# Optimization experiments

Hardware: AMD Instinct MI355X
Metric: run time of the kernel (lower is better)

Reference implementation:

```python
import jax, jax.numpy as jnp
import numpy as np

B, N, DQ, DK, DV, H = 8, 1024, 512, 512, 512, 8
DH = DV // H  # 64


def setup_inputs() -> dict:
    key = jax.random.key(0)
    ks = jax.random.split(key, 12)
    Q = jax.random.normal(ks[0], (B, N, DQ), jnp.float32)
    K = jax.random.normal(ks[1], (B, N, DK), jnp.float32)
    U = jax.random.normal(ks[2], (H, N, N, B), jnp.float32) * 0.1  # additive bias, [H,Nq,Nk,B]
    mask = (jax.random.uniform(ks[3], (B, N)) < 0.9).astype(jnp.float32)
    w = 0.02
    return {
        'Q': Q, 'K': K, 'U': U, 'mask': mask,
        'Wq': jax.random.normal(ks[4], (DQ, DV), jnp.float32) * w,
        'bq': jnp.zeros((DV,), jnp.float32),
        'Wk': jax.random.normal(ks[5], (DK, DV), jnp.float32) * w,
        'bk': jnp.zeros((DV,), jnp.float32),
        'Wv': jax.random.normal(ks[6], (DK, DV), jnp.float32) * w,
        'bv': jnp.zeros((DV,), jnp.float32),
        'Wo': jax.random.normal(ks[7], (DV, DV), jnp.float32) * w,
        'bo': jnp.zeros((DV,), jnp.float32),
    }


def reference(Q, K, U, mask, Wq, bq, Wk, bk, Wv, bv, Wo, bo):
    m = mask[:, :, None]  # [B,N,1]
    q = (Q @ Wq + bq) * m  # [B,N,DV]
    k = (K @ Wk + bk) * m
    v = (K @ Wv + bv) * m
    # split heads: torch.cat(split(dh,2),0) is head-major -> [H,B,N,DH]
    qh = q.reshape(B, N, H, DH).transpose(2, 0, 1, 3)
    kh = k.reshape(B, N, H, DH).transpose(2, 0, 1, 3)
    vh = v.reshape(B, N, H, DH).transpose(2, 0, 1, 3)
    # U.transpose(1,3).transpose(-1,-2).reshape(H*B,N,N) == transpose(U,(0,3,1,2))
    bias = jnp.transpose(U, (0, 3, 1, 2))  # [H,B,Nq,Nk]
    scores = jnp.einsum('hbid,hbjd->hbij', qh, kh) / np.sqrt(DV) + bias
    # custom double-masked softmax (max taken over unmasked scores, faithfully)
    max_elem = jnp.max(scores, axis=3, keepdims=True)
    m1 = mask[None, :, :, None]  # [1,B,Nq,1]
    m2 = mask[None, :, None, :]  # [1,B,1,Nk]
    num = jnp.exp((scores - max_elem) * m1 * m2) * m1 * m2
    A = num / (jnp.sum(num, axis=3, keepdims=True) + 1e-16)
    o = qh + jnp.einsum('hbij,hbjd->hbid', A, vh)  # residual, [H,B,N,DH]
    O = o.transpose(1, 2, 0, 3).reshape(B, N, DV)  # merge heads
    O = O + jax.nn.relu((O @ Wo + bo) * m)
    return O
```

## Files before the change

kernel.cpp:

```cpp
#include <hip/hip_runtime.h>

#define B_   8
#define N_   1024
#define D_   512
#define H_   8
#define DH_  64
#define SCALE_ 0.044194173824159216f
#define LOG2E_ 1.4426950408889634f

typedef __attribute__((ext_vector_type(8))) short bf16x8;
typedef __attribute__((ext_vector_type(4))) float f32x4;
typedef __attribute__((ext_vector_type(8))) unsigned short us8;

__device__ __forceinline__ unsigned short f2bf(float f) {
  unsigned u = __builtin_bit_cast(unsigned, f);
  u += 0x7fffu + ((u >> 16) & 1u);
  return (unsigned short)(u >> 16);
}
__device__ __forceinline__ float bf2f(unsigned short h) {
  unsigned u = ((unsigned)h) << 16;
  return __builtin_bit_cast(float, u);
}
__device__ __forceinline__ void gl_lds16(const void* g, void* l) {
  __builtin_amdgcn_global_load_lds(
      (const __attribute__((address_space(1))) unsigned int*)g,
      (__attribute__((address_space(3))) unsigned int*)l, 16, 0, 0);
}
#define MFMA16(a, b, c) __builtin_amdgcn_mfma_f32_16x16x32_bf16((a), (b), (c), 0, 0, 0)

__global__ void prep_w(const float* __restrict__ Wq, const float* __restrict__ Wk,
                       const float* __restrict__ Wv, const float* __restrict__ Wo,
                       unsigned short* __restrict__ WT) {
  int idx = blockIdx.x * 256 + threadIdx.x;
  int mat = idx >> 18;
  int rem = idx & 0x3FFFF;
  int k = rem >> 9, n = rem & 511;
  const float* W = (mat == 0) ? Wq : (mat == 1) ? Wk : (mat == 2) ? Wv : Wo;
  float v = W[(size_t)k * 512 + n];
  int kmap = (k & ~63) | ((k & 63) ^ ((n & 7) << 3));
  WT[(size_t)mat * 262144 + (size_t)n * 512 + kmap] = f2bf(v);
}

#define GEMM_BODY(A, W, bias, EPILOGUE)                                          \
  __shared__ unsigned short Alds[2][128][72];                                    \
  __shared__ unsigned short Blds[2][128 * 64];                                   \
  const int t = threadIdx.x, w = t >> 6, l = t & 63;                             \
  const int wr = w >> 1, wc = w & 1;                                             \
  const int lm = l & 15, lg = l >> 4;                                            \
  const int bm = blockIdx.x >> 2, bn = blockIdx.x & 3;                           \
  f32x4 acc[4][4];                                                               \
  _Pragma("unroll") for (int mt = 0; mt < 4; ++mt)                               \
  _Pragma("unroll") for (int nt = 0; nt < 4; ++nt)                               \
      acc[mt][nt] = f32x4{0.f, 0.f, 0.f, 0.f};                                   \
  float4 areg[8];                                                                \
  auto loadA = [&](int kt) {                                                     \
    _Pragma("unroll") for (int p = 0; p < 8; ++p) {                              \
      int row = (t >> 4) + p * 16, col = (t & 15) * 4;                           \
      areg[p] = *(const float4*)&A[((size_t)(bm * 128 + row)) * 512 + kt * 64 + col]; \
    }                                                                            \
  };                                                                             \
  auto issueB = [&](int kt, int sb) {                                            \
    _Pragma("unroll") for (int p = 0; p < 4; ++p) {                              \
      int chunk = w * 4 + p;                                                     \
      int row = chunk * 8 + (l >> 3), gc = kt * 64 + (l & 7) * 8;                \
      gl_lds16(&W[((size_t)(bn * 128 + row)) * 512 + gc],                        \
               &Blds[sb][chunk * 512 + l * 8]);                                  \
    }                                                                            \
  };                                                                             \
  auto writeA = [&](int sb) {                                                    \
    _Pragma("unroll") for (int p = 0; p < 8; ++p) {                              \
      int row = (t >> 4) + p * 16, col = (t & 15) * 4;                           \
      float4 v = areg[p];                                                        \
      uint2 d;                                                                   \
      d.x = (unsigned)f2bf(v.x) | ((unsigned)f2bf(v.y) << 16);                   \
      d.y = (unsigned)f2bf(v.z) | ((unsigned)f2bf(v.w) << 16);                   \
      *(uint2*)&Alds[sb][row][col] = d;                                          \
    }                                                                            \
  };                                                                             \
  loadA(0); issueB(0, 0); writeA(0);                                             \
  __syncthreads();                                                               \
  int buf = 0;                                                                   \
  for (int kt = 0; kt < 8; ++kt) {                                               \
    if (kt + 1 < 8) { loadA(kt + 1); issueB(kt + 1, buf ^ 1); }                  \
    _Pragma("unroll") for (int kk = 0; kk < 2; ++kk) {                           \
      bf16x8 af[4], bfv[4];                                                      \
      _Pragma("unroll") for (int mt = 0; mt < 4; ++mt)                           \
        af[mt] = *(const bf16x8*)&Alds[buf][wr * 64 + mt * 16 + lm][kk * 32 + lg * 8]; \
      _Pragma("unroll") for (int nt = 0; nt < 4; ++nt) {                         \
        int rr = wc * 64 + nt * 16 + lm;                                         \
        int c = (kk * 32 + lg * 8) ^ ((rr & 7) << 3);                            \
        bfv[nt] = *(const bf16x8*)&Blds[buf][rr * 64 + c];                       \
      }                                                                          \
      _Pragma("unroll") for (int mt = 0; mt < 4; ++mt)                           \
      _Pragma("unroll") for (int nt = 0; nt < 4; ++nt)                           \
          acc[mt][nt] = MFMA16(af[mt], bfv[nt], acc[mt][nt]);                    \
    }                                                                            \
    if (kt + 1 < 8) writeA(buf ^ 1);                                             \
    __syncthreads();                                                             \
    buf ^= 1;                                                                    \
  }                                                                              \
  _Pragma("unroll") for (int mt = 0; mt < 4; ++mt)                               \
  _Pragma("unroll") for (int nt = 0; nt < 4; ++nt) {                             \
    int gn = bn * 128 + wc * 64 + nt * 16 + lm;                                  \
    float bv_ = bias[gn];                                                        \
    _Pragma("unroll") for (int e = 0; e < 4; ++e) {                              \
      int gm = bm * 128 + wr * 64 + mt * 16 + lg * 4 + e;                        \
      float v = acc[mt][nt][e] + bv_;                                            \
      size_t off = (size_t)gm * 512 + gn;                                        \
      EPILOGUE                                                                   \
    }                                                                            \
  }

__global__ __launch_bounds__(256, 2) void gemm_proj3(
    const float* __restrict__ Q, const float* __restrict__ K,
    const unsigned short* __restrict__ WT,
    const float* __restrict__ bq, const float* __restrict__ bk,
    const float* __restrict__ bv, const float* __restrict__ mask,
    unsigned short* __restrict__ qb, unsigned short* __restrict__ kb,
    unsigned short* __restrict__ vtmp) {
  const int mat = blockIdx.y;
  const float* A = (mat == 0) ? Q : K;
  const unsigned short* W = WT + (size_t)mat * 262144;
  const float* bias = (mat == 0) ? bq : (mat == 1) ? bk : bv;
  unsigned short* outp = (mat == 0) ? qb : (mat == 1) ? kb : vtmp;
  GEMM_BODY(A, W, bias, { outp[off] = f2bf(v * mask[gm]); })
}

__global__ __launch_bounds__(256, 2) void gemm_final(
    const float* __restrict__ A, const unsigned short* __restrict__ W,
    const float* __restrict__ bias, const float* __restrict__ mask,
    const float* __restrict__ resid, float* __restrict__ outp) {
  GEMM_BODY(A, W, bias, { outp[off] = resid[off] + fmaxf(v, 0.f) * mask[gm]; })
}

__global__ void vtrans_kernel(const unsigned short* __restrict__ vtmp,
                              unsigned short* __restrict__ vT) {
  __shared__ unsigned short T[64][72];
  int b = blockIdx.x, ntile = blockIdx.y, dtile = blockIdx.z;
  int n0 = ntile * 64, d0 = dtile * 64;
  int t = threadIdx.x;
#pragma unroll
  for (int p = 0; p < 2; ++p) {
    int r = (t >> 3) + p * 32;
    int c = (t & 7) * 8;
    *(us8*)&T[r][c] = *(const us8*)&vtmp[((size_t)(b * N_ + n0 + r)) * D_ + d0 + c];
  }
  __syncthreads();
#pragma unroll
  for (int p = 0; p < 2; ++p) {
    int r = (t >> 3) + p * 32;
    int c = (t & 7) * 8;
    us8 v;
#pragma unroll
    for (int e = 0; e < 8; ++e) v[e] = T[c + e][r];
    *(us8*)&vT[((size_t)(b * D_ + d0 + r)) * N_ + n0 + c] = v;
  }
}

__global__ __launch_bounds__(512, 2) void attn_kernel(
    const unsigned short* __restrict__ qb, const unsigned short* __restrict__ kb,
    const unsigned short* __restrict__ vT, const float* __restrict__ U,
    const float* __restrict__ mask, float* __restrict__ O32) {
  __shared__ float Ulds[2][32 * 256];
  __shared__ float Plds[8][32 * 36];
  const int t = threadIdx.x, w = t >> 6, l = t & 63;
  const int h = blockIdx.x >> 5;
  const int i0 = (blockIdx.x & 31) * 32;
  const int b = w;
  const int lm = l & 15, lg = l >> 4;
  const int bh = b >> 2;
  const int xw_b = (b & 3) ^ (lm & 3);

  float4 ur[4];
  auto stageLoad = [&](int jt_) {
    const size_t base = (((size_t)h * N_ + i0) * N_ + (size_t)jt_ * 32) * B_;
#pragma unroll
    for (int p = 0; p < 4; ++p)
      ur[p] = *(const float4*)&U[base + (size_t)(w * 4 + p) * (N_ * B_) + l * 4];
  };
  auto stageWrite = [&](int sb) {
    int xw = (l >> 1) & 3;
    int gd = l ^ ((w & 3) << 1);
#pragma unroll
    for (int p = 0; p < 4; ++p) {
      float4 v = ur[p];
      if (xw & 1) v = float4{v.y, v.x, v.w, v.z};
      if (xw & 2) v = float4{v.z, v.w, v.x, v.y};
      *(float4*)&Ulds[sb][(w * 4 + p) * 256 + gd * 4] = v;
    }
  };

  bf16x8 qf[2][2];
#pragma unroll
  for (int mt = 0; mt < 2; ++mt)
#pragma unroll
    for (int kt = 0; kt < 2; ++kt)
      qf[mt][kt] = *(const bf16x8*)&qb[((size_t)(b * N_ + i0 + lm + 16 * mt)) * D_ +
                                       h * DH_ + kt * 32 + lg * 8];

  f32x4 acc[2][4];
#pragma unroll
  for (int mt = 0; mt < 2; ++mt)
#pragma unroll
    for (int nt = 0; nt < 4; ++nt) acc[mt][nt] = f32x4{0.f, 0.f, 0.f, 0.f};
  float lrun[2][4];
#pragma unroll
  for (int mt = 0; mt < 2; ++mt)
#pragma unroll
    for (int e = 0; e < 4; ++e) lrun[mt][e] = 0.f;

  stageLoad(0);
  stageWrite(0);
  __syncthreads();

  for (int jt_ = 0; jt_ < 32; ++jt_) {
    if (jt_ + 1 < 32) stageLoad(jt_ + 1);
    const int buf = jt_ & 1;
    const int j0 = jt_ * 32;

    bf16x8 kf[2][2];
#pragma unroll
    for (int jt = 0; jt < 2; ++jt)
#pragma unroll
      for (int kt = 0; kt < 2; ++kt)
        kf[jt][kt] = *(const bf16x8*)&kb[((size_t)(b * N_ + j0 + lm + 16 * jt)) * D_ +
                                         h * DH_ + kt * 32 + lg * 8];
    bf16x8 vf[4];
#pragma unroll
    for (int nt = 0; nt < 4; ++nt)
      vf[nt] = *(const bf16x8*)&vT[((size_t)(b * D_ + h * DH_ + lm + 16 * nt)) * N_ +
                                   j0 + lg * 8];
    float mj0 = mask[b * N_ + j0 + lm];
    float mj1 = mask[b * N_ + j0 + lm + 16];

    f32x4 S[2][2];
#pragma unroll
    for (int mt = 0; mt < 2; ++mt)
#pragma unroll
      for (int jt = 0; jt < 2; ++jt) {
        f32x4 s = f32x4{0.f, 0.f, 0.f, 0.f};
#pragma unroll
        for (int kt = 0; kt < 2; ++kt) s = MFMA16(qf[mt][kt], kf[jt][kt], s);
        S[mt][jt] = s;
      }

#pragma unroll
    for (int mt = 0; mt < 2; ++mt) {
      const int g0 = ((lm * 2 + bh) ^ (lg << 1));
#pragma unroll
      for (int e = 0; e < 4; ++e) {
        int il = lg * 4 + e + 16 * mt;
        float u0 = Ulds[buf][il * 256 + g0 * 4 + xw_b];
        float u1 = Ulds[buf][il * 256 + (g0 + 32) * 4 + xw_b];
        float s0 = S[mt][0][e] * SCALE_ + u0;
        float s1 = S[mt][1][e] * SCALE_ + u1;
        float p0 = (mj0 != 0.f) ? exp2f(s0 * LOG2E_) : 0.f;
        float p1 = (mj1 != 0.f) ? exp2f(s1 * LOG2E_) : 0.f;
        lrun[mt][e] += p0 + p1;
        Plds[w][il * 36 + lm] = p0;
        Plds[w][il * 36 + lm + 16] = p1;
      }
    }

#pragma unroll
    for (int mt = 0; mt < 2; ++mt) {
      float4 pa0 = *(const float4*)&Plds[w][(lm + 16 * mt) * 36 + lg * 8];
      float4 pa1 = *(const float4*)&Plds[w][(lm + 16 * mt) * 36 + lg * 8 + 4];
      bf16x8 paf;
      paf[0] = (short)f2bf(pa0.x); paf[1] = (short)f2bf(pa0.y);
      paf[2] = (short)f2bf(pa0.z); paf[3] = (short)f2bf(pa0.w);
      paf[4] = (short)f2bf(pa1.x); paf[5] = (short)f2bf(pa1.y);
      paf[6] = (short)f2bf(pa1.z); paf[7] = (short)f2bf(pa1.w);
#pragma unroll
      for (int nt = 0; nt < 4; ++nt)
        acc[mt][nt] = MFMA16(paf, vf[nt], acc[mt][nt]);
    }

    if (jt_ + 1 < 32) stageWrite(buf ^ 1);
    __syncthreads();
  }

#pragma unroll
  for (int mt = 0; mt < 2; ++mt)
#pragma unroll
    for (int e = 0; e < 4; ++e) {
      float lv = lrun[mt][e];
      lv += __shfl_xor(lv, 1);
      lv += __shfl_xor(lv, 2);
      lv += __shfl_xor(lv, 4);
      lv += __shfl_xor(lv, 8);
      lrun[mt][e] = lv;
    }

#pragma unroll
  for (int mt = 0; mt < 2; ++mt)
#pragma unroll
    for (int e = 0; e < 4; ++e) {
      int gi = i0 + lg * 4 + e + 16 * mt;
      float mi = mask[b * N_ + gi];
      float rD = 1.f / (lrun[mt][e] + 1e-16f);
#pragma unroll
      for (int nt = 0; nt < 4; ++nt) {
        int gd = h * DH_ + lm + 16 * nt;
        size_t off = ((size_t)(b * N_ + gi)) * D_ + gd;
        float qv = bf2f(qb[off]);
        O32[off] = mi * (qv + acc[mt][nt][e] * rD);
      }
    }
}

extern "C" void kernel_launch(void* const* d_in, const int* in_sizes, int n_in,
                              void* d_out, int out_size, void* d_ws, size_t ws_size,
                              hipStream_t stream) {
  const float* Q    = (const float*)d_in[0];
  const float* K    = (const float*)d_in[1];
  const float* U    = (const float*)d_in[2];
  const float* mask = (const float*)d_in[3];
  const float* Wq   = (const float*)d_in[4];
  const float* bq   = (const float*)d_in[5];
  const float* Wk   = (const float*)d_in[6];
  const float* bk   = (const float*)d_in[7];
  const float* Wv   = (const float*)d_in[8];
  const float* bv   = (const float*)d_in[9];
  const float* Wo   = (const float*)d_in[10];
  const float* bo   = (const float*)d_in[11];
  float* out = (float*)d_out;

  char* ws = (char*)d_ws;
  unsigned short* WT   = (unsigned short*)ws;
  unsigned short* qb   = (unsigned short*)(ws + (2llu << 20));
  unsigned short* kb   = (unsigned short*)(ws + (10llu << 20));
  unsigned short* vtmp = (unsigned short*)(ws + (18llu << 20));
  unsigned short* vTb  = (unsigned short*)(ws + (26llu << 20));
  float* O32           = (float*)(ws + (34llu << 20));

  prep_w<<<4096, 256, 0, stream>>>(Wq, Wk, Wv, Wo, WT);
  gemm_proj3<<<dim3(256, 3), 256, 0, stream>>>(Q, K, WT, bq, bk, bv, mask, qb, kb, vtmp);
  vtrans_kernel<<<dim3(8, 16, 8), 256, 0, stream>>>(vtmp, vTb);
  attn_kernel<<<256, 512, 0, stream>>>(qb, kb, vTb, U, mask, O32);
  gemm_final<<<256, 256, 0, stream>>>(O32, WT + 3 * 262144, bo, mask, O32, out);
}
```

Measured before the change: 210.2 us.

## Load U bias directly to registers with register double-buffering, halve query tile

The attention kernel no longer stages the bias U through a double-buffered LDS tile with block-wide barriers. Each lane now loads its own U elements straight from global memory into registers, together with K, V and mask fragments, using a two-stage register prefetch. The query tile shrinks from 32 to 16 rows, doubling the grid to 512 blocks, and block indices are remapped so that co-scheduled blocks touch neighbouring regions. The P-to-bf16 conversion uses a packed hardware convert instruction. Scalar strided U loads (stride 8 floats across lanes) may waste memory bandwidth on a bandwidth-bound 256 MB bias read, and K/V fragments are now reread twice as often.

Result: slower. 325.3 us (+54.8%).

```diff
diff --git a/kernel.cpp b/kernel.cpp
--- a/kernel.cpp
+++ b/kernel.cpp
@@ -11,6 +11,7 @@
 typedef __attribute__((ext_vector_type(8))) short bf16x8;
 typedef __attribute__((ext_vector_type(4))) float f32x4;
 typedef __attribute__((ext_vector_type(8))) unsigned short us8;
+typedef __attribute__((ext_vector_type(4))) unsigned int u32x4;
 
 __device__ __forceinline__ unsigned short f2bf(float f) {
   unsigned u = __builtin_bit_cast(unsigned, f);
@@ -25,6 +26,11 @@
   __builtin_amdgcn_global_load_lds(
       (const __attribute__((address_space(1))) unsigned int*)g,
       (__attribute__((address_space(3))) unsigned int*)l, 16, 0, 0);
+}
+__device__ __forceinline__ unsigned cvt_pk_bf16(float lo, float hi) {
+  unsigned r;
+  asm("v_cvt_pk_bf16_f32 %0, %1, %2" : "=v"(r) : "v"(lo), "v"(hi));
+  return r;
 }
 #define MFMA16(a, b, c) __builtin_amdgcn_mfma_f32_16x16x32_bf16((a), (b), (c), 0, 0, 0)
 
@@ -161,152 +167,108 @@
     const unsigned short* __restrict__ qb, const unsigned short* __restrict__ kb,
     const unsigned short* __restrict__ vT, const float* __restrict__ U,
     const float* __restrict__ mask, float* __restrict__ O32) {
-  __shared__ float Ulds[2][32 * 256];
-  __shared__ float Plds[8][32 * 36];
+  __shared__ float Plds[8][16 * 36];
   const int t = threadIdx.x, w = t >> 6, l = t & 63;
-  const int h = blockIdx.x >> 5;
-  const int i0 = (blockIdx.x & 31) * 32;
+  int bid = (int)blockIdx.x;
+  bid = (bid & 7) * 64 + (bid >> 3);
+  const int h = bid >> 6;
+  const int i0 = (bid & 63) * 16;
   const int b = w;
   const int lm = l & 15, lg = l >> 4;
-  const int bh = b >> 2;
-  const int xw_b = (b & 3) ^ (lm & 3);
-
-  float4 ur[4];
-  auto stageLoad = [&](int jt_) {
-    const size_t base = (((size_t)h * N_ + i0) * N_ + (size_t)jt_ * 32) * B_;
-#pragma unroll
-    for (int p = 0; p < 4; ++p)
-      ur[p] = *(const float4*)&U[base + (size_t)(w * 4 + p) * (N_ * B_) + l * 4];
+
+  const float* Ub = U + (((size_t)h * N_ + i0 + lg * 4) * N_ + lm) * B_ + b;
+  const unsigned short* Kb = kb + (size_t)b * N_ * D_ + h * DH_ + lg * 8;
+  const unsigned short* Vb = vT + ((size_t)b * D_ + h * DH_ + lm) * N_ + lg * 8;
+  const float* Mb = mask + b * N_ + lm;
+
+  bf16x8 qf[2];
+#pragma unroll
+  for (int kt = 0; kt < 2; ++kt)
+    qf[kt] = *(const bf16x8*)&qb[((size_t)b * N_ + i0 + lm) * D_ + h * DH_ + kt * 32 + lg * 8];
+
+  f32x4 acc[4];
+#pragma unroll
+  for (int nt = 0; nt < 4; ++nt) acc[nt] = f32x4{0.f, 0.f, 0.f, 0.f};
+  float lrun[4] = {0.f, 0.f, 0.f, 0.f};
+
+  float uA[8], uB[8];
+  bf16x8 kA[2][2], kB[2][2], vA[4], vB[4];
+  float mAv[2], mBv[2];
+
+  auto pref = [&](int jt, float (&u)[8], bf16x8 (&kf)[2][2], bf16x8 (&vf)[4],
+                  float (&mj)[2]) {
+#pragma unroll
+    for (int e = 0; e < 4; ++e) {
+      u[e * 2]     = Ub[(size_t)e * 8192 + jt * 256];
+      u[e * 2 + 1] = Ub[(size_t)e * 8192 + jt * 256 + 128];
+    }
+#pragma unroll
+    for (int j2 = 0; j2 < 2; ++j2)
+#pragma unroll
+      for (int kt = 0; kt < 2; ++kt)
+        kf[j2][kt] = *(const bf16x8*)&Kb[(size_t)(jt * 32 + j2 * 16 + lm) * D_ + kt * 32];
+#pragma unroll
+    for (int nt = 0; nt < 4; ++nt)
+      vf[nt] = *(const bf16x8*)&Vb[(size_t)nt * 16 * N_ + jt * 32];
+    mj[0] = Mb[jt * 32];
+    mj[1] = Mb[jt * 32 + 16];
   };
-  auto stageWrite = [&](int sb) {
-    int xw = (l >> 1) & 3;
-    int gd = l ^ ((w & 3) << 1);
-#pragma unroll
-    for (int p = 0; p < 4; ++p) {
-      float4 v = ur[p];
-      if (xw & 1) v = float4{v.y, v.x, v.w, v.z};
-      if (xw & 2) v = float4{v.z, v.w, v.x, v.y};
-      *(float4*)&Ulds[sb][(w * 4 + p) * 256 + gd * 4] = v;
+
+  auto comp = [&](const float (&u)[8], const bf16x8 (&kf)[2][2], const bf16x8 (&vf)[4],
+                  const float (&mj)[2]) {
+    f32x4 S0 = f32x4{0.f, 0.f, 0.f, 0.f}, S1 = f32x4{0.f, 0.f, 0.f, 0.f};
+#pragma unroll
+    for (int kt = 0; kt < 2; ++kt) {
+      S0 = MFMA16(qf[kt], kf[0][kt], S0);
+      S1 = MFMA16(qf[kt], kf[1][kt], S1);
     }
+#pragma unroll
+    for (int e = 0; e < 4; ++e) {
+      float s0 = S0[e] * SCALE_ + u[e * 2];
+      float s1 = S1[e] * SCALE_ + u[e * 2 + 1];
+      float p0 = (mj[0] != 0.f) ? exp2f(s0 * LOG2E_) : 0.f;
+      float p1 = (mj[1] != 0.f) ? exp2f(s1 * LOG2E_) : 0.f;
+      lrun[e] += p0 + p1;
+      Plds[w][(lg * 4 + e) * 36 + lm] = p0;
+      Plds[w][(lg * 4 + e) * 36 + lm + 16] = p1;
+    }
+    float4 pa0 = *(const float4*)&Plds[w][lm * 36 + lg * 8];
+    float4 pa1 = *(const float4*)&Plds[w][lm * 36 + lg * 8 + 4];
+    u32x4 pk;
+    pk[0] = cvt_pk_bf16(pa0.x, pa0.y);
+    pk[1] = cvt_pk_bf16(pa0.z, pa0.w);
+    pk[2] = cvt_pk_bf16(pa1.x, pa1.y);
+    pk[3] = cvt_pk_bf16(pa1.z, pa1.w);
+    bf16x8 paf = __builtin_bit_cast(bf16x8, pk);
+#pragma unroll
+    for (int nt = 0; nt < 4; ++nt) acc[nt] = MFMA16(paf, vf[nt], acc[nt]);
   };
 
-  bf16x8 qf[2][2];
-#pragma unroll
-  for (int mt = 0; mt < 2; ++mt)
-#pragma unroll
-    for (int kt = 0; kt < 2; ++kt)
-      qf[mt][kt] = *(const bf16x8*)&qb[((size_t)(b * N_ + i0 + lm + 16 * mt)) * D_ +
-                                       h * DH_ + kt * 32 + lg * 8];
-
-  f32x4 acc[2][4];
-#pragma unroll
-  for (int mt = 0; mt < 2; ++mt)
-#pragma unroll
-    for (int nt = 0; nt < 4; ++nt) acc[mt][nt] = f32x4{0.f, 0.f, 0.f, 0.f};
-  float lrun[2][4];
-#pragma unroll
-  for (int mt = 0; mt < 2; ++mt)
-#pragma unroll
-    for (int e = 0; e < 4; ++e) lrun[mt][e] = 0.f;
-
-  stageLoad(0);
-  stageWrite(0);
-  __syncthreads();
-
-  for (int jt_ = 0; jt_ < 32; ++jt_) {
-    if (jt_ + 1 < 32) stageLoad(jt_ + 1);
-    const int buf = jt_ & 1;
-    const int j0 = jt_ * 32;
-
-    bf16x8 kf[2][2];
-#pragma unroll
-    for (int jt = 0; jt < 2; ++jt)
-#pragma unroll
-      for (int kt = 0; kt < 2; ++kt)
-        kf[jt][kt] = *(const bf16x8*)&kb[((size_t)(b * N_ + j0 + lm + 16 * jt)) * D_ +
-                                         h * DH_ + kt * 32 + lg * 8];
-    bf16x8 vf[4];
-#pragma unroll
-    for (int nt = 0; nt < 4; ++nt)
-      vf[nt] = *(const bf16x8*)&vT[((size_t)(b * D_ + h * DH_ + lm + 16 * nt)) * N_ +
-                                   j0 + lg * 8];
-    float mj0 = mask[b * N_ + j0 + lm];
-    float mj1 = mask[b * N_ + j0 + lm + 16];
-
-    f32x4 S[2][2];
-#pragma unroll
-    for (int mt = 0; mt < 2; ++mt)
-#pragma unroll
-      for (int jt = 0; jt < 2; ++jt) {
-        f32x4 s = f32x4{0.f, 0.f, 0.f, 0.f};
-#pragma unroll
-        for (int kt = 0; kt < 2; ++kt) s = MFMA16(qf[mt][kt], kf[jt][kt], s);
-        S[mt][jt] = s;
-      }
-
-#pragma unroll
-    for (int mt = 0; mt < 2; ++mt) {
-      const int g0 = ((lm * 2 + bh) ^ (lg << 1));
-#pragma unroll
-      for (int e = 0; e < 4; ++e) {
-        int il = lg * 4 + e + 16 * mt;
-        float u0 = Ulds[buf][il * 256 + g0 * 4 + xw_b];
-        float u1 = Ulds[buf][il * 256 + (g0 + 32) * 4 + xw_b];
-        float s0 = S[mt][0][e] * SCALE_ + u0;
-        float s1 = S[mt][1][e] * SCALE_ + u1;
-        float p0 = (mj0 != 0.f) ? exp2f(s0 * LOG2E_) : 0.f;
-        float p1 = (mj1 != 0.f) ? exp2f(s1 * LOG2E_) : 0.f;
-        lrun[mt][e] += p0 + p1;
-        Plds[w][il * 36 + lm] = p0;
-        Plds[w][il * 36 + lm + 16] = p1;
-      }
+  pref(0, uA, kA, vA, mAv);
+  for (int jt = 0; jt < 32; jt += 2) {
+    pref(jt + 1, uB, kB, vB, mBv);
+    comp(uA, kA, vA, mAv);
+    if (jt + 2 < 32) pref(jt + 2, uA, kA, vA, mAv);
+    comp(uB, kB, vB, mBv);
+  }
+
+#pragma unroll
+  for (int e = 0; e < 4; ++e) {
+    float lv = lrun[e];
+    lv += __shfl_xor(lv, 1);
+    lv += __shfl_xor(lv, 2);
+    lv += __shfl_xor(lv, 4);
+    lv += __shfl_xor(lv, 8);
+    int gi = i0 + lg * 4 + e;
+    float mi = mask[b * N_ + gi];
+    float rD = 1.f / (lv + 1e-16f);
+#pragma unroll
+    for (int nt = 0; nt < 4; ++nt) {
+      size_t off = ((size_t)b * N_ + gi) * D_ + h * DH_ + lm + nt * 16;
+      float qv = bf2f(qb[off]);
+      O32[off] = mi * (qv + acc[nt][e] * rD);
     }
-
-#pragma unroll
-    for (int mt = 0; mt < 2; ++mt) {
-      float4 pa0 = *(const float4*)&Plds[w][(lm + 16 * mt) * 36 + lg * 8];
-      float4 pa1 = *(const float4*)&Plds[w][(lm + 16 * mt) * 36 + lg * 8 + 4];
-      bf16x8 paf;
-      paf[0] = (short)f2bf(pa0.x); paf[1] = (short)f2bf(pa0.y);
-      paf[2] = (short)f2bf(pa0.z); paf[3] = (short)f2bf(pa0.w);
-      paf[4] = (short)f2bf(pa1.x); paf[5] = (short)f2bf(pa1.y);
-      paf[6] = (short)f2bf(pa1.z); paf[7] = (short)f2bf(pa1.w);
-#pragma unroll
-      for (int nt = 0; nt < 4; ++nt)
-        acc[mt][nt] = MFMA16(paf, vf[nt], acc[mt][nt]);
-    }
-
-    if (jt_ + 1 < 32) stageWrite(buf ^ 1);
-    __syncthreads();
-  }
-
-#pragma unroll
-  for (int mt = 0; mt < 2; ++mt)
-#pragma unroll
-    for (int e = 0; e < 4; ++e) {
-      float lv = lrun[mt][e];
-      lv += __shfl_xor(lv, 1);
-      lv += __shfl_xor(lv, 2);
-      lv += __shfl_xor(lv, 4);
-      lv += __shfl_xor(lv, 8);
-      lrun[mt][e] = lv;
-    }
-
-#pragma unroll
-  for (int mt = 0; mt < 2; ++mt)
-#pragma unroll
-    for (int e = 0; e < 4; ++e) {
-      int gi = i0 + lg * 4 + e + 16 * mt;
-      float mi = mask[b * N_ + gi];
-      float rD = 1.f / (lrun[mt][e] + 1e-16f);
-#pragma unroll
-      for (int nt = 0; nt < 4; ++nt) {
-        int gd = h * DH_ + lm + 16 * nt;
-        size_t off = ((size_t)(b * N_ + gi)) * D_ + gd;
-        float qv = bf2f(qb[off]);
-        O32[off] = mi * (qv + acc[mt][nt][e] * rD);
-      }
-    }
+  }
 }
 
 extern "C" void kernel_launch(void* const* d_in, const int* in_sizes, int n_in,
@@ -337,6 +299,6 @@
   prep_w<<<4096, 256, 0, stream>>>(Wq, Wk, Wv, Wo, WT);
   gemm_proj3<<<dim3(256, 3), 256, 0, stream>>>(Q, K, WT, bq, bk, bv, mask, qb, kb, vtmp);
   vtrans_kernel<<<dim3(8, 16, 8), 256, 0, stream>>>(vtmp, vTb);
-  attn_kernel<<<256, 512, 0, stream>>>(qb, kb, vTb, U, mask, O32);
+  attn_kernel<<<512, 512, 0, stream>>>(qb, kb, vTb, U, mask, O32);
   gemm_final<<<256, 256, 0, stream>>>(O32, WT + 3 * 262144, bo, mask, O32, out);
 }
```
